# Kernel tuning notes

Hardware: AMD Instinct MI355X
Metric: run time of the kernel (lower is better)

## Reference

```python
import jax, jax.numpy as jnp
import numpy as np

B, N, F_IN = 32, 512, 64
HEADS = (8, 8)
HIDS = (64, 64)
EDGE_P = 0.05  # graph density
NEG_SLOPE = 0.2
NEG_INF = -1e20


def setup_inputs() -> dict:
    key = jax.random.key(0)
    ks = jax.random.split(key, 8)
    x = jax.random.normal(ks[0], (B, N, F_IN), dtype=jnp.float32)
    adj = (jax.random.uniform(ks[1], (B, N, N)) < EDGE_P).astype(jnp.float32)
    adj = jnp.maximum(adj, adj.transpose(0, 2, 1))  # symmetric adjacency
    # mask = (batch, row): every (b, n) pair gets the masked softmax
    b_idx = jnp.repeat(jnp.arange(B, dtype=jnp.int32), N)   # [B*N]
    r_idx = jnp.tile(jnp.arange(N, dtype=jnp.int32), B)     # [B*N]
    # layer 0: f_in=64 -> f_out=64, H=8 ; layer 1: f_in=64*8=512 -> f_out=64, H=8
    W0 = jax.random.normal(ks[2], (F_IN, HIDS[0]), dtype=jnp.float32) / jnp.sqrt(jnp.float32(F_IN))
    a_src0 = jax.random.normal(ks[3], (HIDS[0], HEADS[0]), dtype=jnp.float32) / jnp.sqrt(jnp.float32(HIDS[0]))
    a_dst0 = jax.random.normal(ks[4], (HIDS[0], HEADS[0]), dtype=jnp.float32) / jnp.sqrt(jnp.float32(HIDS[0]))
    f_in1 = HIDS[0] * HEADS[0]
    W1 = jax.random.normal(ks[5], (f_in1, HIDS[1]), dtype=jnp.float32) / jnp.sqrt(jnp.float32(f_in1))
    a_src1 = jax.random.normal(ks[6], (HIDS[1], HEADS[1]), dtype=jnp.float32) / jnp.sqrt(jnp.float32(HIDS[1]))
    a_dst1 = jax.random.normal(ks[7], (HIDS[1], HEADS[1]), dtype=jnp.float32) / jnp.sqrt(jnp.float32(HIDS[1]))
    return dict(x=x, adj=adj, b_idx=b_idx, r_idx=r_idx,
                W0=W0, a_src0=a_src0, a_dst0=a_dst0,
                W1=W1, a_src1=a_src1, a_dst1=a_dst1)


def _gat_layer(x, adj, b_idx, r_idx, W, a_src, a_dst):
    # x: [B,N,f_in], adj: [B,N,N] (diag already set), W: [f_in,F], a_*: [F,H]
    hp = x @ W                                        # [B,N,F]
    s = jnp.einsum('bnf,fh->bhn', hp, a_src)          # attn_src
    d = jnp.einsum('bnf,fh->bhn', hp, a_dst)          # attn_dst
    attn = s[:, :, :, None] + d[:, :, None, :]        # [B,H,N,N]
    attn = jnp.where(attn >= 0, attn, NEG_SLOPE * attn)  # leaky_relu(0.2)
    attn = jnp.where(adj[:, None, :, :] == 0, 0.0, attn)  # masked_fill(adj==0, 0)
    rows = attn[b_idx, :, r_idx, :]                   # [K,H,N]
    rows = jnp.where(rows == 0.0, NEG_INF, rows)
    rows = jax.nn.softmax(rows, axis=-1)
    attn = attn.at[b_idx, :, r_idx, :].set(rows)
    return jnp.einsum('bhij,bjf->bhif', attn, hp)     # [B,H,N,F]


def reference(x, adj, b_idx, r_idx, W0, a_src0, a_dst0, W1, a_src1, a_dst1):
    Bn, Nn = x.shape[:2]
    # torch mutates adj in place: adj[batch,row,row] = 1 (self loops)
    adj = adj.at[b_idx, r_idx, r_idx].set(1.0)
    o = _gat_layer(x, adj, b_idx, r_idx, W0, a_src0, a_dst0)      # [B,H,N,F0]
    x1 = jax.nn.elu(o.transpose(0, 2, 1, 3).reshape(Bn, Nn, -1))  # [B,N,H*F0]
    o2 = _gat_layer(x1, adj, b_idx, r_idx, W1, a_src1, a_dst1)    # [B,H,N,F1]
    return o2.mean(axis=1)                                        # [B,N,F1]
```

## Files before the change

kernel.cpp:

```cpp
#include <hip/hip_runtime.h>
#include <hip/hip_bf16.h>
#include <math.h>

#define BB 32
#define NN 512

typedef _Float16 f16x8 __attribute__((ext_vector_type(8)));
typedef __fp16  fp16x2 __attribute__((ext_vector_type(2)));
typedef float f32x4 __attribute__((ext_vector_type(4)));

#define MFMA16(a, b, c) __builtin_amdgcn_mfma_f32_16x16x32_f16(a, b, c, 0, 0, 0)

union AF { f16x8 v; unsigned int u[4]; };

__device__ __forceinline__ void gload_lds16(const void* g, void* l) {
    __builtin_amdgcn_global_load_lds(
        (const __attribute__((address_space(1))) unsigned int*)g,
        (__attribute__((address_space(3))) unsigned int*)l, 16, 0, 0);
}

__global__ __launch_bounds__(256) void k_wt_prep(
    const float* __restrict__ W0, _Float16* __restrict__ W0T,
    const float* __restrict__ W1, _Float16* __restrict__ W1T)
{
    int id = blockIdx.x * 256 + threadIdx.x;
    const float* W; _Float16* WT; int KT, task;
    if (id < 512) { W = W0; WT = W0T; KT = 64;  task = id; }
    else          { W = W1; WT = W1T; KT = 512; task = id - 512; }
    int n = task & 63, gabs = task >> 6;
    int c = gabs >> 3, g = gabs & 7;
    f16x8 hv;
#pragma unroll
    for (int e = 0; e < 8; ++e)
        hv[e] = (_Float16)W[(size_t)(gabs * 8 + e) * 64 + n];
    *(f16x8*)(WT + (size_t)n * KT + c * 64 + (g ^ (n & 7)) * 8) = hv;
}

__global__ __launch_bounds__(256) void k_maxd(
    const float* __restrict__ dTg, float* __restrict__ maxd)
{
    __shared__ float sm[4];
    int bh = blockIdx.x;
    int t = threadIdx.x, lane = t & 63, w = t >> 6;
    const float* p = dTg + (size_t)bh * NN;
    float m = fmaxf(p[t], p[t + 256]);
#pragma unroll
    for (int off = 32; off; off >>= 1) m = fmaxf(m, __shfl_xor(m, off));
    if (lane == 0) sm[w] = m;
    __syncthreads();
    if (t == 0) maxd[bh] = fmaxf(fmaxf(sm[0], sm[1]), fmaxf(sm[2], sm[3]));
}

static __device__ __forceinline__ void epi_sd_hpt(
    const float* ctile, const float* asd_f, int row0, int t,
    float* __restrict__ s, float* __restrict__ dTg, _Float16* __restrict__ hpT)
{
    int b = row0 >> 9, jb = row0 & 511;
    if (t < 128) {
        int rr = t >> 3, h = t & 7;
        float sv = 0.f, dv = 0.f;
#pragma unroll
        for (int f = 0; f < 64; ++f) {
            float hv = ctile[rr * 66 + f];
            sv = fmaf(hv, asd_f[f * 8 + h], sv);
            dv = fmaf(hv, asd_f[512 + f * 8 + h], dv);
        }
        s[((size_t)b * NN + jb + rr) * 8 + h] = sv;
        dTg[((size_t)b * 8 + h) * NN + jb + rr] = dv;
    } else {
        int t2 = t - 128;
        int f = t2 >> 1, jl = (t2 & 1) * 8;
        f16x8 hv;
#pragma unroll
        for (int e = 0; e < 8; ++e)
            hv[e] = (_Float16)ctile[(jl + e) * 66 + f];
        *(f16x8*)(hpT + ((size_t)b * 64 + f) * NN + jb + jl) = hv;
    }
}

__global__ __launch_bounds__(256) void k_gemm0(
    const float* __restrict__ x, const _Float16* __restrict__ W0T,
    const float* __restrict__ a_src, const float* __restrict__ a_dst,
    const float* __restrict__ adj, unsigned long long* __restrict__ adjb,
    float* __restrict__ s, float* __restrict__ dTg, _Float16* __restrict__ hpT)
{
    __shared__ float ctile[16 * 66];
    __shared__ float asd_f[1024];
    __shared__ unsigned int mrow[16][16];
    int t = threadIdx.x, row0 = blockIdx.x * 16;
    int lane = t & 63, w = t >> 6, cn = lane & 15, rq = lane >> 4;

    int ar = t >> 4, seg = t & 15;
    const float* ap = adj + (size_t)(row0 + ar) * NN + seg * 32;
    float4 av[8];
#pragma unroll
    for (int q = 0; q < 8; ++q) av[q] = ((const float4*)ap)[q];

    ((float4*)asd_f)[t] = (t < 128) ? ((const float4*)a_src)[t]
                                    : ((const float4*)a_dst)[t - 128];
    f32x4 acc;
#pragma unroll
    for (int e = 0; e < 4; ++e) acc[e] = 0.f;
#pragma unroll
    for (int ks = 0; ks < 2; ++ks) {
        const float* xp = x + (size_t)(row0 + cn) * 64 + ks * 32 + rq * 8;
        float4 x0 = *(const float4*)xp, x1 = *(const float4*)(xp + 4);
        f16x8 ah = {(_Float16)x0.x, (_Float16)x0.y, (_Float16)x0.z, (_Float16)x0.w,
                    (_Float16)x1.x, (_Float16)x1.y, (_Float16)x1.z, (_Float16)x1.w};
        int nn = w * 16 + cn;
        f16x8 bh = *(const f16x8*)(W0T + (size_t)nn * 64 + (((ks * 4 + rq) ^ (nn & 7)) * 8));
        acc = MFMA16(ah, bh, acc);
    }
#pragma unroll
    for (int r = 0; r < 4; ++r)
        ctile[(rq * 4 + r) * 66 + w * 16 + cn] = acc[r];
    __syncthreads();
    epi_sd_hpt(ctile, asd_f, row0, t, s, dTg, hpT);

    unsigned int m32 = 0;
#pragma unroll
    for (int q = 0; q < 8; ++q) {
        if (av[q].x != 0.f) m32 |= 1u << (q * 4 + 0);
        if (av[q].y != 0.f) m32 |= 1u << (q * 4 + 1);
        if (av[q].z != 0.f) m32 |= 1u << (q * 4 + 2);
        if (av[q].w != 0.f) m32 |= 1u << (q * 4 + 3);
    }
    int i = (row0 + ar) & (NN - 1);
    if ((i >> 5) == seg) m32 |= 1u << (i & 31);
    mrow[ar][seg] = m32;
    __syncthreads();
    if (t < 128) {
        int r = t >> 3, k = t & 7;
        unsigned long long u = (unsigned long long)mrow[r][2 * k]
                             | ((unsigned long long)mrow[r][2 * k + 1] << 32);
        adjb[(size_t)(row0 + r) * 8 + k] = u;
    }
}

#define PSTEP(DD0v, DD1v, MBYTE, KS, HTC)                               \
    do {                                                                \
        AF aA, aB;                                                      \
        _Pragma("unroll")                                               \
        for (int e = 0; e < 8; e += 2) {                                \
            float pA[2], pB[2];                                         \
            _Pragma("unroll")                                           \
            for (int q = 0; q < 2; ++q) {                               \
                int ee = e + q;                                         \
                bool con = (MBYTE >> ee) & 1u;                          \
                float e0 = sv0 + DD0v[ee];                              \
                float l0 = fmaxf(e0, 0.2f * e0);                        \
                float p0 = __expf(l0 - M0);                             \
                pA[q] = (con && l0 != 0.f) ? p0 : 0.f;                  \
                float e1 = sv1 + DD1v[ee];                              \
                float l1 = fmaxf(e1, 0.2f * e1);                        \
                float p1 = __expf(l1 - M1);                             \
                pB[q] = (con && l1 != 0.f) ? p1 : 0.f;                  \
            }                                                           \
            fp16x2 ka = __builtin_amdgcn_cvt_pkrtz(pA[0], pA[1]);       \
            fp16x2 kb = __builtin_amdgcn_cvt_pkrtz(pB[0], pB[1]);       \
            aA.u[e >> 1] = __builtin_bit_cast(unsigned int, ka);        \
            aB.u[e >> 1] = __builtin_bit_cast(unsigned int, kb);        \
        }                                                               \
        accrs[0] = MFMA16(aA.v, ones, accrs[0]);                        \
        accrs[1] = MFMA16(aB.v, ones, accrs[1]);                        \
        _Pragma("unroll")                                               \
        for (int ft = 0; ft < 4; ++ft) {                                \
            int f = ft * 16 + cn;                                       \
            f16x8 bh = *(const f16x8*)&HTC[f * 64 + ((((KS) * 4 + rq) ^ (f & 7)) * 8)]; \
            acc[0][ft] = MFMA16(aA.v, bh, acc[0][ft]);                  \
            acc[1][ft] = MFMA16(aB.v, bh, acc[1][ft]);                  \
        }                                                               \
    } while (0)

#define STAGE_SC(SC, B)                                                  \
    do {                                                                 \
        _Float16* t0_ = (_Float16*)(B) + (w << 9);                       \
        _Float16* t1_ = (_Float16*)((B) + 8192) + (w << 9);              \
        gload_lds16(src0 + (SC) * 128, t0_);                             \
        gload_lds16(src1 + (SC) * 128, t0_ + 2048);                      \
        gload_lds16(src0 + (SC) * 128 + 64, t1_);                        \
        gload_lds16(src1 + (SC) * 128 + 64, t1_ + 2048);                 \
        gload_lds16(dsrc + (SC) * 128, (float*)((B) + 16384) + (w << 8));\
    } while (0)

template<int MODE>
__global__ __launch_bounds__(256, 4) void k_attn_fused(
    const unsigned long long* __restrict__ adjb, const float* __restrict__ s,
    const float* __restrict__ dTg, const float* __restrict__ maxd,
    const _Float16* __restrict__ hpT,
    const _Float16* __restrict__ W1T,
    const float* __restrict__ a_src, const float* __restrict__ a_dst,
    float* __restrict__ s_out, float* __restrict__ dTg_out,
    _Float16* __restrict__ hpT_out, float* __restrict__ o_f)
{
    __shared__ __align__(16) char smem[40960];

    int blk = blockIdx.x;
    int vb = ((blk & 7) << 7) | (blk >> 3);
    int b = vb >> 5, i0 = (vb & 31) << 4;
    int row0 = vb * 16;
    int t = threadIdx.x, lane = t & 63, w = t >> 6;
    int cn = lane & 15, rq = lane >> 4;
    int h0 = 2 * w, h1 = h0 + 1;
    int myrow = i0 + cn;

    const _Float16* hb = hpT + (size_t)b * 64 * NN;
    int f0 = t >> 3, g0 = t & 7;
    const _Float16* src0 = hb + (size_t)f0 * NN + ((g0 ^ (f0 & 7)) * 8);
    const _Float16* src1 = hb + (size_t)(f0 + 32) * NN + ((g0 ^ (f0 & 7)) * 8);
    const float* dgB = dTg + (size_t)b * 8 * NN;
    int hs = h0 + (lane >> 5), js = (lane & 31) * 4;
    const float* dsrc = dgB + (size_t)hs * NN + js;

    char* bufP = smem;
    char* bufQ = smem + 20480;

    STAGE_SC(0, bufP);

    float sv0 = s[((size_t)b * NN + myrow) * 8 + h0];
    float sv1 = s[((size_t)b * NN + myrow) * 8 + h1];
    float M0 = fmaxf(sv0 + maxd[b * 8 + h0], 0.f);
    float M1 = fmaxf(sv1 + maxd[b * 8 + h1], 0.f);
    const unsigned long long* abr = adjb + ((size_t)b * NN + myrow) * 8;
    int rq8 = rq * 8;
    unsigned long long mb0 = abr[0], mb1 = abr[1];

    f16x8 ones;
#pragma unroll
    for (int e = 0; e < 8; ++e) ones[e] = (_Float16)1.0f;

    f32x4 acc[2][4], accrs[2];
#pragma unroll
    for (int hh = 0; hh < 2; ++hh) {
#pragma unroll
        for (int e = 0; e < 4; ++e) accrs[hh][e] = 0.f;
#pragma unroll
        for (int ft = 0; ft < 4; ++ft)
#pragma unroll
            for (int e = 0; e < 4; ++e) acc[hh][ft][e] = 0.f;
    }

    __syncthreads();

    for (int sc = 0; sc < 4; ++sc) {
        char* cur = (sc & 1) ? bufQ : bufP;
        char* nxt = (sc & 1) ? bufP : bufQ;
        if (sc < 3) STAGE_SC(sc + 1, nxt);
        unsigned long long nm0 = 0, nm1 = 0;
        if (sc < 3) { nm0 = abr[2 * sc + 2]; nm1 = abr[2 * sc + 3]; }
        const float* ddl0 = (const float*)(cur + 16384) + h0 * 128;
        const float* ddl1 = ddl0 + 128;
#pragma unroll
        for (int half = 0; half < 2; ++half) {
            unsigned long long mbc = half ? mb1 : mb0;
            unsigned int ml = (unsigned int)mbc, mh = (unsigned int)(mbc >> 32);
            const _Float16* hTc = (const _Float16*)(cur + half * 8192);
#pragma unroll
            for (int ks = 0; ks < 2; ++ks) {
                int jrel = half * 64 + ks * 32 + rq8;
                unsigned int mby = ((ks ? mh : ml) >> rq8) & 0xffu;
                float dd0[8], dd1[8];
                *(float4*)&dd0[0] = *(const float4*)(ddl0 + jrel);
                *(float4*)&dd0[4] = *(const float4*)(ddl0 + jrel + 4);
                *(float4*)&dd1[0] = *(const float4*)(ddl1 + jrel);
                *(float4*)&dd1[4] = *(const float4*)(ddl1 + jrel + 4);
                PSTEP(dd0, dd1, mby, ks, hTc);
            }
        }
        mb0 = nm0; mb1 = nm1;
        __syncthreads();
    }

    float invr[2][4];
#pragma unroll
    for (int hh = 0; hh < 2; ++hh)
#pragma unroll
        for (int r = 0; r < 4; ++r) invr[hh][r] = 1.0f / accrs[hh][r];

    if (MODE == 0) {
        _Float16* x1all = (_Float16*)(smem + 16384);
#pragma unroll
        for (int hh = 0; hh < 2; ++hh) {
            int h = h0 + hh;
#pragma unroll
            for (int ft = 0; ft < 4; ++ft)
#pragma unroll
                for (int r = 0; r < 4; ++r) {
                    int il = rq * 4 + r;
                    float v = acc[hh][ft][r] * invr[hh][r];
                    v = v > 0.f ? v : __expf(v) - 1.f;
                    int f = ft * 16 + cn;
                    x1all[h * 1024 + il * 64 + (((f >> 3) ^ (il & 7)) * 8) + (f & 7)] =
                        (_Float16)v;
                }
        }
        __syncthreads();
        f32x4 g1;
#pragma unroll
        for (int e = 0; e < 4; ++e) g1[e] = 0.f;
        int nn = w * 16 + cn;
        const _Float16* wb = W1T + (size_t)nn * 512;
#pragma unroll
        for (int kc = 0; kc < 8; ++kc) {
#pragma unroll
            for (int ks = 0; ks < 2; ++ks) {
                f16x8 ah = *(const f16x8*)&x1all[kc * 1024 + cn * 64 +
                                                 (((ks * 4 + rq) ^ (cn & 7)) * 8)];
                f16x8 bh = *(const f16x8*)(wb + kc * 64 +
                                           (((ks * 4 + rq) ^ (nn & 7)) * 8));
                g1 = MFMA16(ah, bh, g1);
            }
        }
        __syncthreads();
        float* ctile = (float*)(smem + 16384);
        float* asd_f = (float*)(smem + 24576);
#pragma unroll
        for (int r = 0; r < 4; ++r)
            ctile[(rq * 4 + r) * 66 + w * 16 + cn] = g1[r];
        ((float4*)asd_f)[t] = (t < 128) ? ((const float4*)a_src)[t]
                                        : ((const float4*)a_dst)[t - 128];
        __syncthreads();
        epi_sd_hpt(ctile, asd_f, row0, t, s_out, dTg_out, hpT_out);
    } else {
        float* red = (float*)smem;
#pragma unroll
        for (int ft = 0; ft < 4; ++ft)
#pragma unroll
            for (int r = 0; r < 4; ++r) {
                int il = rq * 4 + r;
                float v = acc[0][ft][r] * invr[0][r]
                        + acc[1][ft][r] * invr[1][r];
                red[(w * 16 + il) * 64 + ft * 16 + cn] = v;
            }
        __syncthreads();
#pragma unroll
        for (int u = 0; u < 4; ++u) {
            int idx = t + u * 256;
            int il = idx >> 6, f = idx & 63;
            float sum = red[il * 64 + f] + red[(16 + il) * 64 + f]
                      + red[(32 + il) * 64 + f] + red[(48 + il) * 64 + f];
            o_f[((size_t)b * NN + i0 + il) * 64 + f] = sum * 0.125f;
        }
    }
}

extern "C" void kernel_launch(void* const* d_in, const int* in_sizes, int n_in,
                              void* d_out, int out_size, void* d_ws, size_t ws_size,
                              hipStream_t stream) {
    const float* x      = (const float*)d_in[0];
    const float* adj    = (const float*)d_in[1];
    const float* W0     = (const float*)d_in[4];
    const float* a_src0 = (const float*)d_in[5];
    const float* a_dst0 = (const float*)d_in[6];
    const float* W1     = (const float*)d_in[7];
    const float* a_src1 = (const float*)d_in[8];
    const float* a_dst1 = (const float*)d_in[9];
    float* out = (float*)d_out;

    float* ws = (float*)d_ws;
    const size_t R = (size_t)BB * NN;
    const size_t BHN = (size_t)BB * 8 * NN;
    float* s0    = ws;
    float* dTg0  = s0 + R * 8;
    float* s1    = dTg0 + BHN;
    float* dTg1  = s1 + R * 8;
    float* maxd0 = dTg1 + BHN;
    float* maxd1 = maxd0 + 256;
    _Float16* hp0T = (_Float16*)(maxd1 + 256);
    _Float16* hp1T = hp0T + (size_t)BB * 64 * NN;
    _Float16* W0T  = hp1T + (size_t)BB * 64 * NN;
    _Float16* W1T  = W0T + (size_t)64 * 64;
    unsigned long long* adjb = (unsigned long long*)(W1T + (size_t)64 * 512);

    k_wt_prep<<<18, 256, 0, stream>>>(W0, W0T, W1, W1T);
    k_gemm0<<<1024, 256, 0, stream>>>(x, W0T, a_src0, a_dst0, adj, adjb,
                                      s0, dTg0, hp0T);
    k_maxd<<<256, 256, 0, stream>>>(dTg0, maxd0);
    k_attn_fused<0><<<1024, 256, 0, stream>>>(adjb, s0, dTg0, maxd0, hp0T,
                                              W1T, a_src1, a_dst1,
                                              s1, dTg1, hp1T, nullptr);
    k_maxd<<<256, 256, 0, stream>>>(dTg1, maxd1);
    k_attn_fused<1><<<1024, 256, 0, stream>>>(adjb, s1, dTg1, maxd1, hp1T,
                                              nullptr, nullptr, nullptr,
                                              nullptr, nullptr, nullptr, out);
}
```

Measured before the change: 156.9 us.

## Fold per-head max into GEMM epilogues via atomics and use one head per wave

Removes the two k_maxd reduction launches. The per-(batch, head) max of the destination scores is now computed in the GEMM epilogues with an order-preserving float encoding and atomicMax, and the buffer is zeroed in the weight-prep kernel. The attention kernel moves to 512 threads, one head per wave, with 64-column chunks over 8 iterations and half the LDS. This cuts per-wave register pressure and raises occupancy, but adds more barriers and a split-K reduction in the layer-1 projection.

```diff
diff --git a/kernel.cpp b/kernel.cpp
--- a/kernel.cpp
+++ b/kernel.cpp
@@ -18,12 +18,27 @@
         (const __attribute__((address_space(1))) unsigned int*)g,
         (__attribute__((address_space(3))) unsigned int*)l, 16, 0, 0);
 }
+__device__ __forceinline__ void gload_lds4(const void* g, void* l) {
+    __builtin_amdgcn_global_load_lds(
+        (const __attribute__((address_space(1))) unsigned int*)g,
+        (__attribute__((address_space(3))) unsigned int*)l, 4, 0, 0);
+}
+
+__device__ __forceinline__ unsigned fenc(float f) {
+    unsigned b = __float_as_uint(f);
+    return (b & 0x80000000u) ? ~b : (b | 0x80000000u);
+}
+__device__ __forceinline__ float fdec(unsigned u) {
+    return __uint_as_float((u & 0x80000000u) ? (u ^ 0x80000000u) : ~u);
+}
 
 __global__ __launch_bounds__(256) void k_wt_prep(
     const float* __restrict__ W0, _Float16* __restrict__ W0T,
-    const float* __restrict__ W1, _Float16* __restrict__ W1T)
+    const float* __restrict__ W1, _Float16* __restrict__ W1T,
+    unsigned* __restrict__ maxdz)
 {
     int id = blockIdx.x * 256 + threadIdx.x;
+    if (id < 512) maxdz[id] = 0u;
     const float* W; _Float16* WT; int KT, task;
     if (id < 512) { W = W0; WT = W0T; KT = 64;  task = id; }
     else          { W = W1; WT = W1T; KT = 512; task = id - 512; }
@@ -36,24 +51,10 @@
     *(f16x8*)(WT + (size_t)n * KT + c * 64 + (g ^ (n & 7)) * 8) = hv;
 }
 
-__global__ __launch_bounds__(256) void k_maxd(
-    const float* __restrict__ dTg, float* __restrict__ maxd)
-{
-    __shared__ float sm[4];
-    int bh = blockIdx.x;
-    int t = threadIdx.x, lane = t & 63, w = t >> 6;
-    const float* p = dTg + (size_t)bh * NN;
-    float m = fmaxf(p[t], p[t + 256]);
-#pragma unroll
-    for (int off = 32; off; off >>= 1) m = fmaxf(m, __shfl_xor(m, off));
-    if (lane == 0) sm[w] = m;
-    __syncthreads();
-    if (t == 0) maxd[bh] = fmaxf(fmaxf(sm[0], sm[1]), fmaxf(sm[2], sm[3]));
-}
-
 static __device__ __forceinline__ void epi_sd_hpt(
     const float* ctile, const float* asd_f, int row0, int t,
-    float* __restrict__ s, float* __restrict__ dTg, _Float16* __restrict__ hpT)
+    float* __restrict__ s, float* __restrict__ dTg, _Float16* __restrict__ hpT,
+    float* dmax_lds, unsigned* __restrict__ maxd_out)
 {
     int b = row0 >> 9, jb = row0 & 511;
     if (t < 128) {
@@ -67,7 +68,8 @@
         }
         s[((size_t)b * NN + jb + rr) * 8 + h] = sv;
         dTg[((size_t)b * 8 + h) * NN + jb + rr] = dv;
-    } else {
+        dmax_lds[t] = dv;
+    } else if (t < 256) {
         int t2 = t - 128;
         int f = t2 >> 1, jl = (t2 & 1) * 8;
         f16x8 hv;
@@ -75,6 +77,13 @@
         for (int e = 0; e < 8; ++e)
             hv[e] = (_Float16)ctile[(jl + e) * 66 + f];
         *(f16x8*)(hpT + ((size_t)b * 64 + f) * NN + jb + jl) = hv;
+    }
+    __syncthreads();
+    if (t < 8) {
+        float m = dmax_lds[t];
+#pragma unroll
+        for (int k = 1; k < 16; ++k) m = fmaxf(m, dmax_lds[t + 8 * k]);
+        atomicMax(maxd_out + (b * 8 + t), fenc(m));
     }
 }
 
@@ -82,11 +91,13 @@
     const float* __restrict__ x, const _Float16* __restrict__ W0T,
     const float* __restrict__ a_src, const float* __restrict__ a_dst,
     const float* __restrict__ adj, unsigned long long* __restrict__ adjb,
-    float* __restrict__ s, float* __restrict__ dTg, _Float16* __restrict__ hpT)
+    float* __restrict__ s, float* __restrict__ dTg, _Float16* __restrict__ hpT,
+    unsigned* __restrict__ maxd)
 {
     __shared__ float ctile[16 * 66];
     __shared__ float asd_f[1024];
     __shared__ unsigned int mrow[16][16];
+    __shared__ float dmax[128];
     int t = threadIdx.x, row0 = blockIdx.x * 16;
     int lane = t & 63, w = t >> 6, cn = lane & 15, rq = lane >> 4;
 
@@ -115,7 +126,7 @@
     for (int r = 0; r < 4; ++r)
         ctile[(rq * 4 + r) * 66 + w * 16 + cn] = acc[r];
     __syncthreads();
-    epi_sd_hpt(ctile, asd_f, row0, t, s, dTg, hpT);
+    epi_sd_hpt(ctile, asd_f, row0, t, s, dTg, hpT, dmax, maxd);
 
     unsigned int m32 = 0;
 #pragma unroll
@@ -137,63 +148,47 @@
     }
 }
 
-#define PSTEP(DD0v, DD1v, MBYTE, KS, HTC)                               \
+#define PSTEP(DDv, MBYTE, KS, HTC)                                      \
     do {                                                                \
-        AF aA, aB;                                                      \
+        AF aA;                                                          \
         _Pragma("unroll")                                               \
         for (int e = 0; e < 8; e += 2) {                                \
-            float pA[2], pB[2];                                         \
+            float pA[2];                                                \
             _Pragma("unroll")                                           \
             for (int q = 0; q < 2; ++q) {                               \
                 int ee = e + q;                                         \
                 bool con = (MBYTE >> ee) & 1u;                          \
-                float e0 = sv0 + DD0v[ee];                              \
+                float e0 = sv + DDv[ee];                                \
                 float l0 = fmaxf(e0, 0.2f * e0);                        \
-                float p0 = __expf(l0 - M0);                             \
+                float p0 = __expf(l0 - M);                              \
                 pA[q] = (con && l0 != 0.f) ? p0 : 0.f;                  \
-                float e1 = sv1 + DD1v[ee];                              \
-                float l1 = fmaxf(e1, 0.2f * e1);                        \
-                float p1 = __expf(l1 - M1);                             \
-                pB[q] = (con && l1 != 0.f) ? p1 : 0.f;                  \
             }                                                           \
             fp16x2 ka = __builtin_amdgcn_cvt_pkrtz(pA[0], pA[1]);       \
-            fp16x2 kb = __builtin_amdgcn_cvt_pkrtz(pB[0], pB[1]);       \
             aA.u[e >> 1] = __builtin_bit_cast(unsigned int, ka);        \
-            aB.u[e >> 1] = __builtin_bit_cast(unsigned int, kb);        \
         }                                                               \
-        accrs[0] = MFMA16(aA.v, ones, accrs[0]);                        \
-        accrs[1] = MFMA16(aB.v, ones, accrs[1]);                        \
+        accrs = MFMA16(aA.v, ones, accrs);                              \
         _Pragma("unroll")                                               \
         for (int ft = 0; ft < 4; ++ft) {                                \
             int f = ft * 16 + cn;                                       \
             f16x8 bh = *(const f16x8*)&HTC[f * 64 + ((((KS) * 4 + rq) ^ (f & 7)) * 8)]; \
-            acc[0][ft] = MFMA16(aA.v, bh, acc[0][ft]);                  \
-            acc[1][ft] = MFMA16(aB.v, bh, acc[1][ft]);                  \
+            acc[ft] = MFMA16(aA.v, bh, acc[ft]);                        \
         }                                                               \
     } while (0)
 
-#define STAGE_SC(SC, B)                                                  \
-    do {                                                                 \
-        _Float16* t0_ = (_Float16*)(B) + (w << 9);                       \
-        _Float16* t1_ = (_Float16*)((B) + 8192) + (w << 9);              \
-        gload_lds16(src0 + (SC) * 128, t0_);                             \
-        gload_lds16(src1 + (SC) * 128, t0_ + 2048);                      \
-        gload_lds16(src0 + (SC) * 128 + 64, t1_);                        \
-        gload_lds16(src1 + (SC) * 128 + 64, t1_ + 2048);                 \
-        gload_lds16(dsrc + (SC) * 128, (float*)((B) + 16384) + (w << 8));\
-    } while (0)
-
 template<int MODE>
-__global__ __launch_bounds__(256, 4) void k_attn_fused(
+__global__ __launch_bounds__(512, 8) void k_attn_fused(
     const unsigned long long* __restrict__ adjb, const float* __restrict__ s,
-    const float* __restrict__ dTg, const float* __restrict__ maxd,
+    const float* __restrict__ dTg, const unsigned* __restrict__ maxd,
     const _Float16* __restrict__ hpT,
     const _Float16* __restrict__ W1T,
     const float* __restrict__ a_src, const float* __restrict__ a_dst,
     float* __restrict__ s_out, float* __restrict__ dTg_out,
-    _Float16* __restrict__ hpT_out, float* __restrict__ o_f)
+    _Float16* __restrict__ hpT_out, unsigned* __restrict__ maxd_out,
+    float* __restrict__ o_f)
 {
-    __shared__ __align__(16) char smem[40960];
+    __shared__ __align__(16) char smem[20480];
+    char* bufP = smem;
+    char* bufQ = smem + 10240;
 
     int blk = blockIdx.x;
     int vb = ((blk & 7) << 7) | (blk >> 3);
@@ -201,107 +196,89 @@
     int row0 = vb * 16;
     int t = threadIdx.x, lane = t & 63, w = t >> 6;
     int cn = lane & 15, rq = lane >> 4;
-    int h0 = 2 * w, h1 = h0 + 1;
     int myrow = i0 + cn;
 
     const _Float16* hb = hpT + (size_t)b * 64 * NN;
     int f0 = t >> 3, g0 = t & 7;
-    const _Float16* src0 = hb + (size_t)f0 * NN + ((g0 ^ (f0 & 7)) * 8);
-    const _Float16* src1 = hb + (size_t)(f0 + 32) * NN + ((g0 ^ (f0 & 7)) * 8);
-    const float* dgB = dTg + (size_t)b * 8 * NN;
-    int hs = h0 + (lane >> 5), js = (lane & 31) * 4;
-    const float* dsrc = dgB + (size_t)hs * NN + js;
-
-    char* bufP = smem;
-    char* bufQ = smem + 20480;
-
-    STAGE_SC(0, bufP);
-
-    float sv0 = s[((size_t)b * NN + myrow) * 8 + h0];
-    float sv1 = s[((size_t)b * NN + myrow) * 8 + h1];
-    float M0 = fmaxf(sv0 + maxd[b * 8 + h0], 0.f);
-    float M1 = fmaxf(sv1 + maxd[b * 8 + h1], 0.f);
+    const _Float16* hsrc = hb + (size_t)f0 * NN + ((g0 ^ (f0 & 7)) * 8);
+    const float* dsrc = dTg + ((size_t)b * 8 + w) * NN + lane;
+
+    {
+        gload_lds16(hsrc, (_Float16*)bufP + (w << 9));
+        gload_lds4(dsrc, (float*)(bufP + 8192) + (w << 6));
+    }
+
+    float sv = s[((size_t)b * NN + myrow) * 8 + w];
+    float md = fdec(maxd[b * 8 + w]);
+    float M = fmaxf(sv + md, 0.f);
     const unsigned long long* abr = adjb + ((size_t)b * NN + myrow) * 8;
     int rq8 = rq * 8;
-    unsigned long long mb0 = abr[0], mb1 = abr[1];
 
     f16x8 ones;
 #pragma unroll
     for (int e = 0; e < 8; ++e) ones[e] = (_Float16)1.0f;
 
-    f32x4 acc[2][4], accrs[2];
-#pragma unroll
-    for (int hh = 0; hh < 2; ++hh) {
-#pragma unroll
-        for (int e = 0; e < 4; ++e) accrs[hh][e] = 0.f;
+    f32x4 acc[4], accrs;
+#pragma unroll
+    for (int e = 0; e < 4; ++e) accrs[e] = 0.f;
+#pragma unroll
+    for (int ft = 0; ft < 4; ++ft)
+#pragma unroll
+        for (int e = 0; e < 4; ++e) acc[ft][e] = 0.f;
+
+    unsigned long long mb = abr[0];
+    __syncthreads();
+
+    for (int jcx = 0; jcx < 8; ++jcx) {
+        int jc = jcx * 64;
+        char* cur = (jcx & 1) ? bufQ : bufP;
+        char* nxt = (jcx & 1) ? bufP : bufQ;
+        if (jcx < 7) {
+            gload_lds16(hsrc + jc + 64, (_Float16*)nxt + (w << 9));
+            gload_lds4(dsrc + jc + 64, (float*)(nxt + 8192) + (w << 6));
+        }
+        unsigned long long mbn = (jcx < 7) ? abr[jcx + 1] : 0ull;
+        const _Float16* hTc = (const _Float16*)cur;
+        const float* ddl = (const float*)(cur + 8192) + (w << 6);
+        unsigned int ml = (unsigned int)mb, mh = (unsigned int)(mb >> 32);
+#pragma unroll
+        for (int ks = 0; ks < 2; ++ks) {
+            float dd[8];
+            *(float4*)&dd[0] = *(const float4*)(ddl + ks * 32 + rq8);
+            *(float4*)&dd[4] = *(const float4*)(ddl + ks * 32 + rq8 + 4);
+            unsigned int mby = ((ks ? mh : ml) >> rq8) & 0xffu;
+            PSTEP(dd, mby, ks, hTc);
+        }
+        mb = mbn;
+        __syncthreads();
+    }
+
+    float invr[4];
+#pragma unroll
+    for (int r = 0; r < 4; ++r) invr[r] = 1.0f / accrs[r];
+
+    if (MODE == 0) {
+        _Float16* x1all = (_Float16*)smem;
 #pragma unroll
         for (int ft = 0; ft < 4; ++ft)
 #pragma unroll
-            for (int e = 0; e < 4; ++e) acc[hh][ft][e] = 0.f;
-    }
-
-    __syncthreads();
-
-    for (int sc = 0; sc < 4; ++sc) {
-        char* cur = (sc & 1) ? bufQ : bufP;
-        char* nxt = (sc & 1) ? bufP : bufQ;
-        if (sc < 3) STAGE_SC(sc + 1, nxt);
-        unsigned long long nm0 = 0, nm1 = 0;
-        if (sc < 3) { nm0 = abr[2 * sc + 2]; nm1 = abr[2 * sc + 3]; }
-        const float* ddl0 = (const float*)(cur + 16384) + h0 * 128;
-        const float* ddl1 = ddl0 + 128;
-#pragma unroll
-        for (int half = 0; half < 2; ++half) {
-            unsigned long long mbc = half ? mb1 : mb0;
-            unsigned int ml = (unsigned int)mbc, mh = (unsigned int)(mbc >> 32);
-            const _Float16* hTc = (const _Float16*)(cur + half * 8192);
-#pragma unroll
-            for (int ks = 0; ks < 2; ++ks) {
-                int jrel = half * 64 + ks * 32 + rq8;
-                unsigned int mby = ((ks ? mh : ml) >> rq8) & 0xffu;
-                float dd0[8], dd1[8];
-                *(float4*)&dd0[0] = *(const float4*)(ddl0 + jrel);
-                *(float4*)&dd0[4] = *(const float4*)(ddl0 + jrel + 4);
-                *(float4*)&dd1[0] = *(const float4*)(ddl1 + jrel);
-                *(float4*)&dd1[4] = *(const float4*)(ddl1 + jrel + 4);
-                PSTEP(dd0, dd1, mby, ks, hTc);
+            for (int r = 0; r < 4; ++r) {
+                int il = rq * 4 + r;
+                float v = acc[ft][r] * invr[r];
+                v = v > 0.f ? v : __expf(v) - 1.f;
+                int f = ft * 16 + cn;
+                x1all[w * 1024 + il * 64 + (((f >> 3) ^ (il & 7)) * 8) + (f & 7)] =
+                    (_Float16)v;
             }
-        }
-        mb0 = nm0; mb1 = nm1;
-        __syncthreads();
-    }
-
-    float invr[2][4];
-#pragma unroll
-    for (int hh = 0; hh < 2; ++hh)
-#pragma unroll
-        for (int r = 0; r < 4; ++r) invr[hh][r] = 1.0f / accrs[hh][r];
-
-    if (MODE == 0) {
-        _Float16* x1all = (_Float16*)(smem + 16384);
-#pragma unroll
-        for (int hh = 0; hh < 2; ++hh) {
-            int h = h0 + hh;
-#pragma unroll
-            for (int ft = 0; ft < 4; ++ft)
-#pragma unroll
-                for (int r = 0; r < 4; ++r) {
-                    int il = rq * 4 + r;
-                    float v = acc[hh][ft][r] * invr[hh][r];
-                    v = v > 0.f ? v : __expf(v) - 1.f;
-                    int f = ft * 16 + cn;
-                    x1all[h * 1024 + il * 64 + (((f >> 3) ^ (il & 7)) * 8) + (f & 7)] =
-                        (_Float16)v;
-                }
-        }
         __syncthreads();
         f32x4 g1;
 #pragma unroll
         for (int e = 0; e < 4; ++e) g1[e] = 0.f;
-        int nn = w * 16 + cn;
+        int nn = (w & 3) * 16 + cn, kh = w >> 2;
         const _Float16* wb = W1T + (size_t)nn * 512;
 #pragma unroll
-        for (int kc = 0; kc < 8; ++kc) {
+        for (int kc2 = 0; kc2 < 4; ++kc2) {
+            int kc = kh * 4 + kc2;
 #pragma unroll
             for (int ks = 0; ks < 2; ++ks) {
                 f16x8 ah = *(const f16x8*)&x1all[kc * 1024 + cn * 64 +
@@ -312,33 +289,43 @@
             }
         }
         __syncthreads();
-        float* ctile = (float*)(smem + 16384);
-        float* asd_f = (float*)(smem + 24576);
+        float* ct = (float*)smem;
+        float* asd_f = (float*)(smem + 12288);
+        float* dmax = (float*)(smem + 16384);
 #pragma unroll
         for (int r = 0; r < 4; ++r)
-            ctile[(rq * 4 + r) * 66 + w * 16 + cn] = g1[r];
-        ((float4*)asd_f)[t] = (t < 128) ? ((const float4*)a_src)[t]
-                                        : ((const float4*)a_dst)[t - 128];
-        __syncthreads();
-        epi_sd_hpt(ctile, asd_f, row0, t, s_out, dTg_out, hpT_out);
+            ct[kh * 1056 + (rq * 4 + r) * 66 + nn] = g1[r];
+        if (t < 256)
+            ((float4*)asd_f)[t] = (t < 128) ? ((const float4*)a_src)[t]
+                                            : ((const float4*)a_dst)[t - 128];
+        __syncthreads();
+        for (int idx = t; idx < 1056; idx += 512) ct[idx] += ct[1056 + idx];
+        __syncthreads();
+        epi_sd_hpt(ct, asd_f, row0, t, s_out, dTg_out, hpT_out, dmax, maxd_out);
     } else {
         float* red = (float*)smem;
 #pragma unroll
-        for (int ft = 0; ft < 4; ++ft)
-#pragma unroll
-            for (int r = 0; r < 4; ++r) {
-                int il = rq * 4 + r;
-                float v = acc[0][ft][r] * invr[0][r]
-                        + acc[1][ft][r] * invr[1][r];
-                red[(w * 16 + il) * 64 + ft * 16 + cn] = v;
+        for (int ph = 0; ph < 2; ++ph) {
+            if ((w >> 2) == ph) {
+#pragma unroll
+                for (int ft = 0; ft < 4; ++ft)
+#pragma unroll
+                    for (int r = 0; r < 4; ++r) {
+                        int il = rq * 4 + r;
+                        float v = acc[ft][r] * invr[r];
+                        int off = (w & 3) * 1024 + il * 64 + ft * 16 + cn;
+                        if (ph == 0) red[off] = v;
+                        else         red[off] += v;
+                    }
             }
-        __syncthreads();
-#pragma unroll
-        for (int u = 0; u < 4; ++u) {
-            int idx = t + u * 256;
+            __syncthreads();
+        }
+#pragma unroll
+        for (int u = 0; u < 2; ++u) {
+            int idx = t + u * 512;
             int il = idx >> 6, f = idx & 63;
-            float sum = red[il * 64 + f] + red[(16 + il) * 64 + f]
-                      + red[(32 + il) * 64 + f] + red[(48 + il) * 64 + f];
+            float sum = red[il * 64 + f] + red[1024 + il * 64 + f]
+                      + red[2048 + il * 64 + f] + red[3072 + il * 64 + f];
             o_f[((size_t)b * NN + i0 + il) * 64 + f] = sum * 0.125f;
         }
     }
@@ -364,23 +351,21 @@
     float* dTg0  = s0 + R * 8;
     float* s1    = dTg0 + BHN;
     float* dTg1  = s1 + R * 8;
-    float* maxd0 = dTg1 + BHN;
-    float* maxd1 = maxd0 + 256;
+    unsigned* maxd0 = (unsigned*)(dTg1 + BHN);
+    unsigned* maxd1 = maxd0 + 256;
     _Float16* hp0T = (_Float16*)(maxd1 + 256);
     _Float16* hp1T = hp0T + (size_t)BB * 64 * NN;
     _Float16* W0T  = hp1T + (size_t)BB * 64 * NN;
     _Float16* W1T  = W0T + (size_t)64 * 64;
     unsigned long long* adjb = (unsigned long long*)(W1T + (size_t)64 * 512);
 
-    k_wt_prep<<<18, 256, 0, stream>>>(W0, W0T, W1, W1T);
+    k_wt_prep<<<18, 256, 0, stream>>>(W0, W0T, W1, W1T, maxd0);
     k_gemm0<<<1024, 256, 0, stream>>>(x, W0T, a_src0, a_dst0, adj, adjb,
-                                      s0, dTg0, hp0T);
-    k_maxd<<<256, 256, 0, stream>>>(dTg0, maxd0);
-    k_attn_fused<0><<<1024, 256, 0, stream>>>(adjb, s0, dTg0, maxd0, hp0T,
+                                      s0, dTg0, hp0T, maxd0);
+    k_attn_fused<0><<<1024, 512, 0, stream>>>(adjb, s0, dTg0, maxd0, hp0T,
                                               W1T, a_src1, a_dst1,
-                                              s1, dTg1, hp1T, nullptr);
-    k_maxd<<<256, 256, 0, stream>>>(dTg1, maxd1);
-    k_attn_fused<1><<<1024, 256, 0, stream>>>(adjb, s1, dTg1, maxd1, hp1T,
+                                              s1, dTg1, hp1T, maxd1, nullptr);
+    k_attn_fused<1><<<1024, 512, 0, stream>>>(adjb, s1, dTg1, maxd1, hp1T,
                                               nullptr, nullptr, nullptr,
-                                              nullptr, nullptr, nullptr, out);
-}
+                                              nullptr, nullptr, nullptr, nullptr, out);
+}
```

Measured after the change: 160.0 us. No clear change (+1.9%).
